# Kernel tuning notes

Hardware: AMD Instinct MI355X
Metric: run time of the kernel (lower is better)

The kernel has to match this reference:

```python
import jax, jax.numpy as jnp
import numpy as np

IMAGES_PER_GPU = 2
IMAGE_MAX_DIM = 1024.0
POOL_SIZE = 7
NUM_ROIS = 1000


def crop_and_resize_level(fm0, boxes, pool_size):
    """TF-style crop_and_resize (bilinear, extrapolation_value=0).
    fm0: [C,H,W] feature map of image 0 (box_indices are all zero in the source).
    boxes: [N,4] normalized (y1,x1,y2,x2).
    returns crops: [N,C,pool_size,pool_size]
    """
    C, H, W = fm0.shape
    P = pool_size
    y1, x1, y2, x2 = boxes[:, 0], boxes[:, 1], boxes[:, 2], boxes[:, 3]
    t = jnp.arange(P, dtype=fm0.dtype) / (P - 1)  # [P]
    # sample coords in source pixel space: [N,P]
    ys = (y1[:, None] + t[None, :] * (y2 - y1)[:, None]) * (H - 1)
    xs = (x1[:, None] + t[None, :] * (x2 - x1)[:, None]) * (W - 1)
    valid_y = (ys >= 0) & (ys <= H - 1)
    valid_x = (xs >= 0) & (xs <= W - 1)
    ysc = jnp.clip(ys, 0.0, H - 1)
    xsc = jnp.clip(xs, 0.0, W - 1)
    y0 = jnp.floor(ysc).astype(jnp.int32)
    x0 = jnp.floor(xsc).astype(jnp.int32)
    y1i = jnp.minimum(y0 + 1, H - 1)
    x1i = jnp.minimum(x0 + 1, W - 1)
    ly = (ysc - y0)  # [N,P]
    lx = (xsc - x0)  # [N,P]

    def g(yi, xi):
        # advanced indexing broadcast -> [C,N,P,P]
        return fm0[:, yi[:, :, None], xi[:, None, :]]

    tl = g(y0, x0)
    tr = g(y0, x1i)
    bl = g(y1i, x0)
    br = g(y1i, x1i)
    lx_b = lx[None, :, None, :]
    ly_b = ly[None, :, :, None]
    top = tl + (tr - tl) * lx_b
    bot = bl + (br - bl) * lx_b
    out = top + (bot - top) * ly_b  # [C,N,P,P]
    mask = (valid_y[:, :, None] & valid_x[:, None, :])  # [N,P,P]
    out = out * mask[None].astype(out.dtype)
    return jnp.transpose(out, (1, 0, 2, 3))  # [N,C,P,P]


def roi_align(feature_maps, rois_flat, pool_size):
    """feature_maps: list of 4 arrays [B,256,Hl,Wl] for levels 2..5.
    rois_flat: [N,4] pixel coords (x1,y1,x2,y2). Returns [N,256,P,P]."""
    x1, y1, x2, y2 = rois_flat[:, 0], rois_flat[:, 1], rois_flat[:, 2], rois_flat[:, 3]
    area = (y2 - y1) * (x2 - x1)
    roi_level = jnp.log2(jnp.sqrt(jnp.maximum(area, 0.0)) / 224.0)
    roi_level = jnp.clip(jnp.round(roi_level) + 4, 2, 5)
    # boxes normalized and reordered (x1,y1,x2,y2) -> (y1,x1,y2,x2)
    boxes = rois_flat[:, jnp.array([1, 0, 3, 2])] / IMAGE_MAX_DIM
    N = rois_flat.shape[0]
    C = feature_maps[0].shape[1]
    pooled = jnp.zeros((N, C, pool_size, pool_size), dtype=feature_maps[0].dtype)
    for i, level in enumerate(range(2, 6)):
        crops = crop_and_resize_level(feature_maps[i][0], boxes, pool_size)
        sel = (roi_level == level)[:, None, None, None]
        pooled = jnp.where(sel, crops, pooled)
    return pooled


def setup_inputs() -> dict:
    key = jax.random.key(0)
    k2, k3, k4, k5, kxy, kwh = jax.random.split(key, 6)
    B, R = IMAGES_PER_GPU, NUM_ROIS
    p2 = jax.random.normal(k2, (B, 256, 256, 256), dtype=jnp.float32)
    p3 = jax.random.normal(k3, (B, 256, 128, 128), dtype=jnp.float32)
    p4 = jax.random.normal(k4, (B, 256, 64, 64), dtype=jnp.float32)
    p5 = jax.random.normal(k5, (B, 256, 32, 32), dtype=jnp.float32)
    xy1 = jax.random.uniform(kxy, (B, R, 2), minval=0.0, maxval=1000.0)
    wh = jax.random.uniform(kwh, (B, R, 2), minval=8.0, maxval=512.0)
    xy2 = jnp.clip(xy1 + wh, 0.0, IMAGE_MAX_DIM)
    rois = jnp.concatenate([xy1, xy2], axis=-1).astype(jnp.float32)  # (x1,y1,x2,y2)
    return {"p2": p2, "p3": p3, "p4": p4, "p5": p5, "rois": rois}


def reference(p2, p3, p4, p5, rois):
    B, R = rois.shape[0], rois.shape[1]
    rois_flat = rois.reshape(B * R, 4)
    pooled = roi_align([p2, p3, p4, p5], rois_flat, POOL_SIZE)
    return pooled.reshape(B, R, 256, POOL_SIZE, POOL_SIZE)
```

## Files before the change

### kernel.cpp

```cpp
#include <hip/hip_runtime.h>

#define P 7
#define PP 49
#define CMAX 256
#define G 8
#define CSPLIT 8
#define CSLICE 32
#define NBINS 256
#define CHUNK 8

#define WS_PERM   2560

typedef float f2 __attribute__((ext_vector_type(2), aligned(4)));

struct PixParam { int o00, o10; float w00, w01, w10, w11; };

__device__ __forceinline__ int roi_level(float x1, float y1, float x2, float y2) {
    const float area = __fmul_rn(__fsub_rn(y2, y1), __fsub_rn(x2, x1));
    int lvl = (int)rintf(log2f(sqrtf(fmaxf(area, 0.0f)) / 224.0f)) + 4;
    return lvl < 2 ? 2 : (lvl > 5 ? 5 : lvl);
}

__global__ __launch_bounds__(256) void prep_kernel(
    const float* __restrict__ rois, int n, unsigned* __restrict__ ws)
{
    __shared__ unsigned s_hist[NBINS];
    __shared__ unsigned s_cur[NBINS];
    const int t = threadIdx.x;
    s_hist[t] = 0u;
    __syncthreads();

    unsigned bloc[8];
    #pragma unroll
    for (int i = 0; i < 8; ++i) {
        const int r = t + i * 256;
        bloc[i] = 0u;
        if (r < n) {
            const float x1 = rois[r*4+0], y1 = rois[r*4+1];
            const float x2 = rois[r*4+2], y2 = rois[r*4+3];
            const int lvl = roi_level(x1, y1, x2, y2);
            int cx = ((int)(__fmul_rn(__fadd_rn(x1, x2), 0.5f))) >> 7; cx = min(cx, 7);
            int cy = ((int)(__fmul_rn(__fadd_rn(y1, y2), 0.5f))) >> 7; cy = min(cy, 7);
            const unsigned b = (unsigned)(((lvl - 2) << 6) | (cy << 3) | cx);
            bloc[i] = b;
            atomicAdd(&s_hist[b], 1u);
        }
    }
    __syncthreads();

    const unsigned h = s_hist[t];
    s_cur[t] = h;
    __syncthreads();
    for (int off = 1; off < NBINS; off <<= 1) {
        const unsigned v = (t >= off) ? s_cur[t - off] : 0u;
        __syncthreads();
        s_cur[t] += v;
        __syncthreads();
    }
    s_cur[t] -= h;
    __syncthreads();

    #pragma unroll
    for (int i = 0; i < 8; ++i) {
        const int r = t + i * 256;
        if (r < n) {
            const unsigned pos = atomicAdd(&s_cur[bloc[i]], 1u);
            ws[WS_PERM + pos] = (unsigned)r;
        }
    }
}

__global__ __launch_bounds__(256) void roialign_main(
    const float* __restrict__ p2, const float* __restrict__ p3,
    const float* __restrict__ p4, const float* __restrict__ p5,
    const float* __restrict__ rois, const unsigned* __restrict__ ws,
    float* __restrict__ out, int n)
{
    __shared__ PixParam sp[G * PP];
    __shared__ const float* fm_s[G];
    __shared__ int hw_s[G];
    __shared__ int H_s[G];
    __shared__ long long obase_s[G];
    __shared__ float box_s[G][4];

    const int nclust = (n + G - 1) / G;

    const int pb  = blockIdx.x;
    const int xcd = pb & 7, j = pb >> 3;
    const int chunk = (j >> 6) * 8 + xcd;
    const int within = j & 63;
    const int cl = chunk * CHUNK + (within & 7);
    const int cb = within >> 3;
    if (cl >= nclust) return;
    const int t  = threadIdx.x;

    if (t < G) {
        const int gi = cl * G + t;
        long long ob = -1; const float* fm = p2; int H = 4; int hw = 0;
        float bx1 = 0.f, by1 = 0.f, bx2 = 0.f, by2 = 0.f;
        if (gi < n) {
            const int rr = (int)ws[WS_PERM + gi];
            bx1 = rois[rr*4+0]; by1 = rois[rr*4+1];
            bx2 = rois[rr*4+2]; by2 = rois[rr*4+3];
            const int lvl = roi_level(bx1, by1, bx2, by2);
            H = 1024 >> lvl;
            hw = H * H;
            fm = (lvl == 2) ? p2 : (lvl == 3) ? p3 : (lvl == 4) ? p4 : p5;
            ob = (long long)rr * (CMAX * PP);
        }
        fm_s[t] = fm; hw_s[t] = hw; H_s[t] = H; obase_s[t] = ob;
        box_s[t][0] = bx1; box_s[t][1] = by1; box_s[t][2] = bx2; box_s[t][3] = by2;
    }
    __syncthreads();

    for (int idx = t; idx < G * PP; idx += 256) {
        const int g = idx / PP, pix = idx % PP;
        PixParam pp; pp.o00 = 0; pp.o10 = 0;
        pp.w00 = 0.f; pp.w01 = 0.f; pp.w10 = 0.f; pp.w11 = 0.f;
        if (obase_s[g] >= 0) {
            const float x1 = box_s[g][0], y1 = box_s[g][1];
            const float x2 = box_s[g][2], y2 = box_s[g][3];
            const int H = H_s[g];
            const int py = pix / P, px = pix % P;
            const float inv = 1.0f / 1024.0f;
            const float by1 = __fmul_rn(y1, inv), bx1 = __fmul_rn(x1, inv);
            const float by2 = __fmul_rn(y2, inv), bx2 = __fmul_rn(x2, inv);
            const float Hm1 = (float)(H - 1);
            const float ty = (float)py / 6.0f;
            const float tx = (float)px / 6.0f;
            const float vy = __fmul_rn(__fadd_rn(by1, __fmul_rn(ty, __fsub_rn(by2, by1))), Hm1);
            const float vx = __fmul_rn(__fadd_rn(bx1, __fmul_rn(tx, __fsub_rn(bx2, bx1))), Hm1);
            const bool vldy = (vy >= 0.0f) && (vy <= Hm1);
            const bool vldx = (vx >= 0.0f) && (vx <= Hm1);
            const float yc = fminf(fmaxf(vy, 0.0f), Hm1);
            const float xc = fminf(fmaxf(vx, 0.0f), Hm1);
            const int y0 = (int)floorf(yc);
            const int x0 = (int)floorf(xc);
            const int y1i = min(y0 + 1, H - 1);
            const float ly = __fsub_rn(yc, (float)y0);
            const float lx = __fsub_rn(xc, (float)x0);
            const float m = (vldy && vldx) ? 1.0f : 0.0f;
            const float wy0 = m * (1.0f - ly), wy1 = m * ly;
            const float wx0 = 1.0f - lx,      wx1 = lx;
            pp.o00 = y0 * H + x0;
            pp.o10 = y1i * H + x0;
            pp.w00 = wy0 * wx0;  pp.w01 = wy0 * wx1;
            pp.w10 = wy1 * wx0;  pp.w11 = wy1 * wx1;
        }
        sp[idx] = pp;
    }
    __syncthreads();

    const int w    = t >> 6;
    const int lane = t & 63;
    const int pix  = lane < PP ? lane : PP - 1;
    const bool act = (lane < PP);

    for (int g = 0; g < G; ++g) {
        const PixParam pp = sp[g * PP + pix];
        const float* fm = fm_s[g];
        const int hw = hw_s[g];
        const long long obg = obase_s[g];
        const int cbase = cb * CSLICE + w * 8;

        f2 tp[8], bt[8];
        #pragma unroll
        for (int k = 0; k < 8; ++k) {
            const float* fmc = fm + (size_t)(cbase + k) * hw;
            tp[k] = *(const f2*)(fmc + pp.o00);
            bt[k] = *(const f2*)(fmc + pp.o10);
        }
        #pragma unroll
        for (int k = 0; k < 8; ++k) {
            const float v = tp[k].x * pp.w00 + tp[k].y * pp.w01
                          + bt[k].x * pp.w10 + bt[k].y * pp.w11;
            if (act && obg >= 0) {
                out[obg + (long long)(cbase + k) * PP + pix] = v;
            }
        }
    }
}

extern "C" void kernel_launch(void* const* d_in, const int* in_sizes, int n_in,
                              void* d_out, int out_size, void* d_ws, size_t ws_size,
                              hipStream_t stream) {
    const float* p2   = (const float*)d_in[0];
    const float* p3   = (const float*)d_in[1];
    const float* p4   = (const float*)d_in[2];
    const float* p5   = (const float*)d_in[3];
    const float* rois = (const float*)d_in[4];
    float* out = (float*)d_out;
    unsigned* ws = (unsigned*)d_ws;
    const int n = in_sizes[4] / 4;

    prep_kernel<<<1, 256, 0, stream>>>(rois, n, ws);

    const int nclust  = (n + G - 1) / G;
    const int nchunk  = (nclust + CHUNK - 1) / CHUNK;
    const int nchunk8 = (nchunk + 7) & ~7;
    const int nblocks = nchunk8 * CHUNK * CSPLIT;
    roialign_main<<<nblocks, 256, 0, stream>>>(p2, p3, p4, p5, rois, ws, out, n);
}
```

Before: 301.1 us.

## Stage ROI bounding window into LDS per channel and interpolate from shared memory

Instead of each lane gathering two float2 taps per channel straight from global memory, each wave cooperatively loads the ROI's bounding pixel window (as float4 chunks) into a per-wave LDS buffer for each channel, then computes the bilinear taps from LDS. The loads for the next channel, and the next ROI's state, are issued ahead in a software-pipelined double-buffer pattern. The aim is coalesced global reads and reuse of shared pixels across sampled points. The cost is extra LDS traffic, more register state, and clamped overreads. There is no barrier between the LDS write and the read within the wave, so correctness depends on the lanes of a wave executing in lockstep. Large boxes can exceed the 320-chunk buffer.

```diff
diff --git a/kernel.cpp b/kernel.cpp
--- a/kernel.cpp
+++ b/kernel.cpp
@@ -8,12 +8,14 @@
 #define CSLICE 32
 #define NBINS 256
 #define CHUNK 8
+#define BUFCH 320
 
 #define WS_PERM   2560
 
-typedef float f2 __attribute__((ext_vector_type(2), aligned(4)));
-
-struct PixParam { int o00, o10; float w00, w01, w10, w11; };
+typedef float f4a4  __attribute__((ext_vector_type(4), aligned(4)));
+typedef float f4a16 __attribute__((ext_vector_type(4), aligned(16)));
+
+struct PixParam { int x0, y0; float w00, w01, w10, w11; };
 
 __device__ __forceinline__ int roi_level(float x1, float y1, float x2, float y2) {
     const float area = __fmul_rn(__fsub_rn(y2, y1), __fsub_rn(x2, x1));
@@ -70,6 +72,18 @@
     }
 }
 
+struct GState {
+    const float* fm;
+    int hw, H, tot, NC, W4x4, offmax, chbase;
+    long long ob;
+    int o0, o1, o2, o3, o4;
+    int tA, tB;
+    float w00, w01, w10, w11;
+    int outb;
+};
+
+struct C5 { f4a4 c0, c1, c2, c3, c4; };
+
 __global__ __launch_bounds__(256) void roialign_main(
     const float* __restrict__ p2, const float* __restrict__ p3,
     const float* __restrict__ p4, const float* __restrict__ p5,
@@ -82,17 +96,18 @@
     __shared__ int H_s[G];
     __shared__ long long obase_s[G];
     __shared__ float box_s[G][4];
+    __shared__ float lbuf[4][BUFCH * 4];
 
     const int nclust = (n + G - 1) / G;
 
     const int pb  = blockIdx.x;
-    const int xcd = pb & 7, j = pb >> 3;
-    const int chunk = (j >> 6) * 8 + xcd;
-    const int within = j & 63;
+    const int xcd = pb & 7, jb = pb >> 3;
+    const int chunk = (jb >> 6) * 8 + xcd;
+    const int within = jb & 63;
     const int cl = chunk * CHUNK + (within & 7);
     const int cb = within >> 3;
     if (cl >= nclust) return;
-    const int t  = threadIdx.x;
+    const int t = threadIdx.x;
 
     if (t < G) {
         const int gi = cl * G + t;
@@ -115,7 +130,7 @@
 
     for (int idx = t; idx < G * PP; idx += 256) {
         const int g = idx / PP, pix = idx % PP;
-        PixParam pp; pp.o00 = 0; pp.o10 = 0;
+        PixParam pp; pp.x0 = 0; pp.y0 = 0;
         pp.w00 = 0.f; pp.w01 = 0.f; pp.w10 = 0.f; pp.w11 = 0.f;
         if (obase_s[g] >= 0) {
             const float x1 = box_s[g][0], y1 = box_s[g][1];
@@ -136,48 +151,112 @@
             const float xc = fminf(fmaxf(vx, 0.0f), Hm1);
             const int y0 = (int)floorf(yc);
             const int x0 = (int)floorf(xc);
-            const int y1i = min(y0 + 1, H - 1);
             const float ly = __fsub_rn(yc, (float)y0);
             const float lx = __fsub_rn(xc, (float)x0);
             const float m = (vldy && vldx) ? 1.0f : 0.0f;
             const float wy0 = m * (1.0f - ly), wy1 = m * ly;
             const float wx0 = 1.0f - lx,      wx1 = lx;
-            pp.o00 = y0 * H + x0;
-            pp.o10 = y1i * H + x0;
+            pp.x0 = x0;  pp.y0 = y0;
             pp.w00 = wy0 * wx0;  pp.w01 = wy0 * wx1;
             pp.w10 = wy1 * wx0;  pp.w11 = wy1 * wx1;
         }
         sp[idx] = pp;
     }
-    __syncthreads();
 
     const int w    = t >> 6;
     const int lane = t & 63;
     const int pix  = lane < PP ? lane : PP - 1;
     const bool act = (lane < PP);
-
+    float* lb = &lbuf[w][0];
+    const int chb0 = cb * CSLICE + w * 8;
+
+    {
+        f4a16 z = {0.f, 0.f, 0.f, 0.f};
+        #pragma unroll
+        for (int ic = 0; ic < 5; ++ic)
+            *(f4a16*)(lb + (lane + ic * 64) * 4) = z;
+    }
+    __syncthreads();
+
+    auto load_g = [&](int g) {
+        GState s;
+        s.fm = fm_s[g]; s.hw = hw_s[g]; s.H = H_s[g]; s.ob = obase_s[g];
+        const int xlo = sp[g*PP + 0].x0, ylo = sp[g*PP + 0].y0;
+        const int x6  = sp[g*PP + 6].x0, y42 = sp[g*PP + 42].y0;
+        const int H = s.H;
+        const int xhi = min(x6 + 1, H - 1), yhi = min(y42 + 1, H - 1);
+        const int Wr = xhi - xlo + 1, Hr = yhi - ylo + 1;
+        const int W4 = (Wr + 3) >> 2;
+        s.W4x4 = W4 << 2;
+        s.tot = Hr * W4;
+        s.NC = (s.tot + 63) >> 6;
+        s.offmax = max(512 * s.hw - 4, 0);
+        s.chbase = chb0 * s.hw;
+        const int gbase = ylo * H + xlo;
+        const float fr = 1.0f / (float)W4;
+        #define CHUNK_OFF(IC, DST) { \
+            int ci = min(lane + IC * 64, s.tot - 1); \
+            int rr = (int)((float)ci * fr); \
+            int rm = ci - rr * W4; \
+            if (rm >= W4) { rm -= W4; ++rr; } else if (rm < 0) { rm += W4; --rr; } \
+            DST = gbase + rr * H + (rm << 2); }
+        CHUNK_OFF(0, s.o0) CHUNK_OFF(1, s.o1) CHUNK_OFF(2, s.o2)
+        CHUNK_OFF(3, s.o3) CHUNK_OFF(4, s.o4)
+        #undef CHUNK_OFF
+        const PixParam pp = sp[g*PP + pix];
+        const int xl = pp.x0 - xlo, yl = pp.y0 - ylo;
+        const int yb = min(pp.y0 + 1, H - 1) - ylo;
+        s.tA = yl * s.W4x4 + xl;
+        s.tB = yb * s.W4x4 + xl;
+        s.w00 = pp.w00; s.w01 = pp.w01; s.w10 = pp.w10; s.w11 = pp.w11;
+        s.outb = (int)s.ob + chb0 * PP + pix;
+        return s;
+    };
+
+    auto issue = [&](const GState& s, int j, C5& c) {
+        const int choff = s.chbase + j * s.hw;
+        if (0 < s.NC) c.c0 = *(const f4a4*)(s.fm + min(choff + s.o0, s.offmax));
+        if (1 < s.NC) c.c1 = *(const f4a4*)(s.fm + min(choff + s.o1, s.offmax));
+        if (2 < s.NC) c.c2 = *(const f4a4*)(s.fm + min(choff + s.o2, s.offmax));
+        if (3 < s.NC) c.c3 = *(const f4a4*)(s.fm + min(choff + s.o3, s.offmax));
+        if (4 < s.NC) c.c4 = *(const f4a4*)(s.fm + min(choff + s.o4, s.offmax));
+    };
+
+    auto write_lds = [&](const GState& s, const C5& c) {
+        if (0 < s.NC) *(f4a16*)(lb + min(lane,           s.tot - 1) * 4) = c.c0;
+        if (1 < s.NC) *(f4a16*)(lb + min(lane + 64,      s.tot - 1) * 4) = c.c1;
+        if (2 < s.NC) *(f4a16*)(lb + min(lane + 128,     s.tot - 1) * 4) = c.c2;
+        if (3 < s.NC) *(f4a16*)(lb + min(lane + 192,     s.tot - 1) * 4) = c.c3;
+        if (4 < s.NC) *(f4a16*)(lb + min(lane + 256,     s.tot - 1) * 4) = c.c4;
+    };
+
+    auto taps_store = [&](const GState& s, int j) {
+        const float t0 = lb[s.tA], t1 = lb[s.tA + 1];
+        const float b0 = lb[s.tB], b1 = lb[s.tB + 1];
+        const float v = t0 * s.w00 + t1 * s.w01 + b0 * s.w10 + b1 * s.w11;
+        if (act && s.ob >= 0) out[s.outb + j * PP] = v;
+    };
+
+    GState A = load_g(0), B;
+    C5 cA, cB;
+    issue(A, 0, cA);
     for (int g = 0; g < G; ++g) {
-        const PixParam pp = sp[g * PP + pix];
-        const float* fm = fm_s[g];
-        const int hw = hw_s[g];
-        const long long obg = obase_s[g];
-        const int cbase = cb * CSLICE + w * 8;
-
-        f2 tp[8], bt[8];
         #pragma unroll
-        for (int k = 0; k < 8; ++k) {
-            const float* fmc = fm + (size_t)(cbase + k) * hw;
-            tp[k] = *(const f2*)(fmc + pp.o00);
-            bt[k] = *(const f2*)(fmc + pp.o10);
-        }
-        #pragma unroll
-        for (int k = 0; k < 8; ++k) {
-            const float v = tp[k].x * pp.w00 + tp[k].y * pp.w01
-                          + bt[k].x * pp.w10 + bt[k].y * pp.w11;
-            if (act && obg >= 0) {
-                out[obg + (long long)(cbase + k) * PP + pix] = v;
+        for (int jj = 0; jj < 4; ++jj) {
+            const int je = jj * 2, jo = je + 1;
+            issue(A, jo, cB);
+            write_lds(A, cA);
+            taps_store(A, je);
+            if (jo < 7) {
+                issue(A, jo + 1, cA);
+            } else if (g + 1 < G) {
+                B = load_g(g + 1);
+                issue(B, 0, cA);
             }
-        }
+            write_lds(A, cB);
+            taps_store(A, jo);
+        }
+        if (g + 1 < G) A = B;
     }
 }
 
```

Result: slower. 403.5 us (+34.0%).
